# Optimization experiments

Hardware: AMD Instinct MI355X
Metric: run time of the kernel (lower is better)

Reference implementation:

```python
import jax, jax.numpy as jnp
import numpy as np
from jax import lax

SEQ_LEN = 12
E = 64        # embedding_dim
HD = 128      # h_dim
G = 32        # number of scenes (seq_start_end rows)
P = 32        # pedestrians per scene
B = G * P     # total batch
BOT = 1024    # bottleneck_dim
MLP = 1024    # mlp_dim
BN_S = 1.0 / np.sqrt(1.0 + 1e-5)  # eval BatchNorm1d with running mean 0 / var 1


def setup_inputs():
    key = jax.random.key(0)
    ks = jax.random.split(key, 32)
    r = lambda k, s, sc=0.1: (jax.random.normal(k, s, jnp.float32) * sc)
    starts = np.arange(G, dtype=np.int32) * P
    sse = jnp.asarray(np.stack([starts, starts + P], 1))
    return {
        'last_pos': r(ks[0], (B, 2), 1.0),
        'last_pos_rel': r(ks[1], (B, 2), 1.0),
        'h0': r(ks[2], (1, B, HD), 1.0),
        'c0': r(ks[3], (1, B, HD), 1.0),
        'vx': r(ks[4], (8, B), 1.0),
        'vy': r(ks[5], (8, B), 1.0),
        'agent_type': jax.random.uniform(ks[6], (8, B, 1), jnp.float32),
        'seq_start_end': sse,
        # decoder params
        'W_sp': r(ks[7], (2, E)), 'b_sp': r(ks[8], (E,)),
        'W_ih': r(ks[9], (E, 4 * HD)), 'W_hh': r(ks[10], (HD, 4 * HD)),
        'b_ih': r(ks[11], (4 * HD,)), 'b_hh': r(ks[12], (4 * HD,)),
        'W_h2p': r(ks[13], (HD, 2)), 'b_h2p': r(ks[14], (2,)),
        # AttenPoolNet params
        'Wp_sp': r(ks[15], (2, E)), 'bp_sp': r(ks[16], (E,)),
        'Wp_vel': r(ks[17], (2, E)), 'bp_vel': r(ks[18], (E,)),
        'Wp_at': r(ks[19], (6, E)), 'bp_at': r(ks[20], (E,)),
        'Wa1': r(ks[21], (E, MLP)), 'ba1': r(ks[22], (MLP,)),
        'Wa2': r(ks[23], (MLP, 1)), 'ba2': r(ks[24], (1,)),
        'Wm1': r(ks[25], (E + HD, 512)), 'bm1': r(ks[26], (512,)),
        'Wm2': r(ks[27], (512, BOT)), 'bm2': r(ks[28], (BOT,)),
        # decoder post-pool mlp: [h+bottleneck, mlp_dim, h]
        'Wd1': r(ks[29], (HD + BOT, MLP)), 'bd1': r(ks[30], (MLP,)),
        'Wd2': r(ks[31], (MLP, HD)), 'bd2': jnp.zeros((HD,), jnp.float32),
    }


def _bnrelu(x):
    # make_mlp: Linear -> BatchNorm1d (eval, mean 0 / var 1) -> ReLU
    return jax.nn.relu(x * BN_S)


def reference(last_pos, last_pos_rel, h0, c0, vx, vy, agent_type, seq_start_end,
              W_sp, b_sp, W_ih, W_hh, b_ih, b_hh, W_h2p, b_h2p,
              Wp_sp, bp_sp, Wp_vel, bp_vel, Wp_at, bp_at,
              Wa1, ba1, Wa2, ba2, Wm1, bm1, Wm2, bm2,
              Wd1, bd1, Wd2, bd2):
    g = seq_start_end.shape[0]
    p = last_pos.shape[0] // g

    at0 = agent_type[0].reshape(g, p, 1)               # agent_type[0,:,:] per group
    at_rep = jnp.repeat(at0, 6, axis=-1)               # .repeat(num_ped, 6) width expansion
    at_emb = at_rep @ Wp_at + bp_at                    # (g,p,E), index j (tiled over i)
    vel = jnp.stack([vx[-1], vy[-1]], -1).reshape(g, p, 2)
    _vel_emb = vel @ Wp_vel + bp_vel                   # computed in source, unused downstream

    def pool(h2d, pos):
        Hh = h2d.reshape(g, p, HD)
        pg = pos.reshape(g, p, 2)
        # rel[s,i,j] = pos[s,j] - pos[s,i]
        rel = pg[:, None, :, :] - pg[:, :, None, :]
        rel_emb = rel @ Wp_sp + bp_sp                  # (g,p,p,E)
        a = _bnrelu(rel_emb @ Wa1 + ba1)               # (g,p,p,MLP)
        s = _bnrelu(a @ Wa2 + ba2)                     # (g,p,p,1)
        w = jax.nn.softmax(s, axis=-1)                 # torch softmax(dim=1) over size-1 axis -> ones
        base = jnp.concatenate([Hh, at_emb], -1)       # (g,p,192), index j
        wt = base[:, None, :, :] * (0.05 * w)          # (g,p,p,192)
        m = _bnrelu(wt @ Wm1 + bm1)
        m = _bnrelu(m @ Wm2 + bm2)                     # (g,p,p,BOT)
        return m.max(axis=2).reshape(g * p, BOT)       # max over j per tile index i

    def lstm(x, h, c):
        gates = x @ W_ih + h @ W_hh + b_ih + b_hh
        i, f, gg, o = jnp.split(gates, 4, axis=-1)
        c = jax.nn.sigmoid(f) * c + jax.nn.sigmoid(i) * jnp.tanh(gg)
        h = jax.nn.sigmoid(o) * jnp.tanh(c)
        return h, c

    def step(carry, _):
        lp, di, h, c = carry
        h, c = lstm(di, h, c)
        rel = h @ W_h2p + b_h2p
        cur = rel + lp
        ph = pool(h, cur)
        dh = _bnrelu(jnp.concatenate([h, ph], -1) @ Wd1 + bd1)
        dh = _bnrelu(dh @ Wd2 + bd2)
        di = rel @ W_sp + b_sp
        return (cur, di, dh, c), rel

    init = (last_pos, last_pos_rel @ W_sp + b_sp, h0[0], c0[0])
    (lp, di, h, c), rels = lax.scan(step, init, None, length=SEQ_LEN)
    return rels, h[None]  # (seq_len,B,2), (1,B,HD)
```

## Files before the change

kernel.cpp:

```cpp
#include <hip/hip_runtime.h>
#include <math.h>

#define BN_SF 0.9999950000374997f

typedef __attribute__((ext_vector_type(8))) short short8v;
typedef __attribute__((ext_vector_type(4))) float float4v;

__device__ __forceinline__ float sigm(float x) { return 1.0f / (1.0f + expf(-x)); }

__device__ __forceinline__ short f2bf(float x) {
    unsigned u = __builtin_bit_cast(unsigned, x);
    unsigned r = (u + 0x7fffu + ((u >> 16) & 1u)) >> 16;
    return (short)r;
}
__device__ __forceinline__ float bf2f(short h) {
    unsigned u = ((unsigned)(unsigned short)h) << 16;
    return __builtin_bit_cast(float, u);
}

template <int K, int N>
__device__ __forceinline__ void cvtB8(const float* __restrict__ src, short* __restrict__ dst,
                                      float scale, int g) {
    const int KCN = K >> 5;
    int ntg = g / (KCN * 64);
    int rem = g - ntg * (KCN * 64);
    int kc = rem >> 6, lane = rem & 63;
    int n = ntg * 16 + (lane & 15);
    int k0 = kc * 32 + ((lane >> 4) << 3);
    short8v v;
#pragma unroll
    for (int j = 0; j < 8; ++j) v[j] = f2bf(scale * src[(size_t)(k0 + j) * N + n]);
    *(short8v*)(dst + (size_t)g * 8) = v;
}

struct SetupP {
    const float *Wm2, *Wd1, *Wd2, *Wm1, *Wih, *Whh, *Wpat, *bpat, *bm1;
    const float *lpr, *Wsp, *bsp, *c0;
    short *Wm2s, *Wd1f, *Wd2f, *Wm1f, *WgHi, *WgLo;
    float *uv, *di, *cbuf;
};

__global__ __launch_bounds__(256) void k_setup(SetupP p) {
    int gt = blockIdx.x * 256 + threadIdx.x;
    int stride = gridDim.x * 256;
    for (int g = gt; g < 512 * 1024 / 8; g += stride)  cvtB8<512, 1024>(p.Wm2, p.Wm2s, 1.f, g);
    for (int g = gt; g < 1152 * 1024 / 8; g += stride) cvtB8<1152, 1024>(p.Wd1, p.Wd1f, 1.f, g);
    for (int g = gt; g < 1024 * 128 / 8; g += stride)  cvtB8<1024, 128>(p.Wd2, p.Wd2f, 1.f, g);
    for (int g = gt; g < 128 * 512 / 8; g += stride)   cvtB8<128, 512>(p.Wm1, p.Wm1f, 0.05f, g);
    for (int g = gt; g < 192 * 512 / 8; g += stride) {
        int ntg = g / (6 * 64);
        int rem = g - ntg * (6 * 64);
        int kc = rem >> 6, lane = rem & 63;
        int n = ntg * 16 + (lane & 15);
        int k0 = kc * 32 + ((lane >> 4) << 3);
        short8v vh, vl;
#pragma unroll
        for (int j = 0; j < 8; ++j) {
            int k = k0 + j;
            float v = (k < 64) ? p.Wih[(size_t)k * 512 + n] : p.Whh[(size_t)(k - 64) * 512 + n];
            short hi = f2bf(v);
            vh[j] = hi; vl[j] = f2bf(v - bf2f(hi));
        }
        *(short8v*)(p.WgHi + (size_t)g * 8) = vh;
        *(short8v*)(p.WgLo + (size_t)g * 8) = vl;
    }
    for (int i = gt; i < 1024 * 64; i += stride) {
        int r = i >> 6, c = i & 63;
        p.di[i] = p.lpr[r * 2] * p.Wsp[c] + p.lpr[r * 2 + 1] * p.Wsp[64 + c] + p.bsp[c];
    }
    for (int i = gt; i < 1024 * 128; i += stride) p.cbuf[i] = p.c0[i];
    if (blockIdx.x == 0) {
        __shared__ float rw[64];
        int t = threadIdx.x;
        if (t < 64) { float s = 0.f; for (int k = 0; k < 6; ++k) s += p.Wpat[k * 64 + t]; rw[t] = s; }
        __syncthreads();
        for (int c = t; c < 512; c += 256) {
            float u = 0.f, v = 0.f;
            for (int e = 0; e < 64; ++e) {
                float wg = p.Wm1[(128 + e) * 512 + c];
                u += rw[e] * wg; v += p.bpat[e] * wg;
            }
            p.uv[c] = 0.05f * u; p.uv[512 + c] = 0.05f * v + p.bm1[c];
        }
    }
}

__global__ __launch_bounds__(512, 4) void k_step(
    const short* __restrict__ WgHi, const short* __restrict__ WgLo,
    const short* __restrict__ Wm1f, const short* __restrict__ Wd2f,
    const short* __restrict__ Wd1f,
    const float* __restrict__ bih, const float* __restrict__ bhh,
    const float* __restrict__ Whp, const float* __restrict__ bhp,
    const float* __restrict__ Wsp, const float* __restrict__ bsp,
    const float* __restrict__ bd1, const float* __restrict__ bd2,
    const float* __restrict__ at0, const float* __restrict__ uv,
    const float* __restrict__ h0,
    const float* __restrict__ phwp, const short* __restrict__ hf_in, int first,
    float* __restrict__ cbuf, float* __restrict__ di,
    short* __restrict__ hf_out, short* __restrict__ m1s,
    float* __restrict__ outrel) {
    __shared__ float sgu[16 * 512];
    __shared__ float sh[16][128];
    __shared__ float sdi[16][64];
    __shared__ float phws[1024];
    __shared__ short xfh[6 * 512];
    __shared__ short xfl[6 * 512];
    __shared__ short xm[4 * 512];
    __shared__ float sat[16];
    __shared__ float srel[16][2];
    short* dh1L = (short*)sgu;
    float* sg = sgu;

    int t = threadIdx.x, b = blockIdx.x;
    int l = t & 63, w = t >> 6;
    int s = b >> 1, mt = b & 1, r0 = b * 16;
    int rbase = (l >> 4) << 2;

    for (int i = t; i < 16 * 64; i += 512) sdi[i >> 6][i & 63] = di[r0 * 64 + i];
    if (t < 16) sat[t] = at0[r0 + t];

    if (first) {
        for (int i = t; i < 16 * 128; i += 512) sh[i >> 7][i & 127] = h0[r0 * 128 + i];
        __syncthreads();
    } else {
        for (int i = t; i < 1024; i += 512) {
            float v = bd1[i];
#pragma unroll
            for (int ct = 0; ct < 8; ++ct) v += phwp[(size_t)s * 8192 + ct * 1024 + i];
            phws[i] = v;
        }
        __syncthreads();
        short8v Ah[4];
#pragma unroll
        for (int kc = 0; kc < 4; ++kc)
            Ah[kc] = *(const short8v*)(hf_in + (size_t)b * 2048 + kc * 512 + l * 8);
#pragma unroll 1
        for (int q2 = 0; q2 < 4; ++q2) {
            short8v B[2][4];
#pragma unroll
            for (int qq = 0; qq < 2; ++qq)
#pragma unroll
                for (int kc = 0; kc < 4; ++kc)
                    B[qq][kc] = *(const short8v*)(Wd1f + (size_t)(w * 8 + q2 * 2 + qq) * 18432 + kc * 512 + l * 8);
            float4v acc2[2];
#pragma unroll
            for (int qq = 0; qq < 2; ++qq) {
                int col = (w * 8 + q2 * 2 + qq) * 16 + (l & 15);
                float pv = phws[col];
                acc2[qq] = (float4v){pv, pv, pv, pv};
            }
#pragma unroll
            for (int kc = 0; kc < 4; ++kc)
#pragma unroll
                for (int qq = 0; qq < 2; ++qq)
                    acc2[qq] = __builtin_amdgcn_mfma_f32_16x16x32_bf16(Ah[kc], B[qq][kc], acc2[qq], 0, 0, 0);
#pragma unroll
            for (int qq = 0; qq < 2; ++qq) {
                int col = (w * 8 + q2 * 2 + qq) * 16 + (l & 15);
                int kcD = col >> 5, jD = col & 7, lD = ((col & 31) >> 3) << 4;
#pragma unroll
                for (int r = 0; r < 4; ++r) {
                    float v = fmaxf(BN_SF * acc2[qq][r], 0.f);
                    dh1L[kcD * 512 + (rbase + r + lD) * 8 + jD] = f2bf(v);
                }
            }
        }
        __syncthreads();
        float4v hacc = {0.f, 0.f, 0.f, 0.f};
        const short* ap = dh1L + l * 8;
        const short* bp = Wd2f + (size_t)w * 16384 + l * 8;
#pragma unroll 1
        for (int kt = 0; kt < 4; ++kt) {
            short8v B[8], A[8];
#pragma unroll
            for (int kk = 0; kk < 8; ++kk) B[kk] = *(const short8v*)(bp + (kt * 8 + kk) * 512);
#pragma unroll
            for (int kk = 0; kk < 8; ++kk) A[kk] = *(const short8v*)(ap + (kt * 8 + kk) * 512);
#pragma unroll
            for (int kk = 0; kk < 8; ++kk)
                hacc = __builtin_amdgcn_mfma_f32_16x16x32_bf16(A[kk], B[kk], hacc, 0, 0, 0);
        }
        int col = w * 16 + (l & 15);
        float bb2 = bd2[col];
        __syncthreads();
#pragma unroll
        for (int r = 0; r < 4; ++r)
            sh[rbase + r][col] = fmaxf(BN_SF * (hacc[r] + bb2), 0.f);
        __syncthreads();
    }

    for (int i = t; i < 6 * 512; i += 512) {
        int pos = i & 511, kc = i >> 9;
        int ll = pos >> 3, j = pos & 7;
        int row = ll & 15, k = kc * 32 + ((ll >> 4) << 3) + j;
        float v = (k < 64) ? sdi[row][k] : sh[row][k - 64];
        short hi = f2bf(v);
        xfh[i] = hi;
        xfl[i] = f2bf(v - bf2f(hi));
    }
    __syncthreads();

    {
        float4v ga[4] = {{0,0,0,0},{0,0,0,0},{0,0,0,0},{0,0,0,0}};
#pragma unroll 1
        for (int kt = 0; kt < 3; ++kt) {
            short8v BH[2][4], BL[2][4], AH[2], AL[2];
#pragma unroll
            for (int kk = 0; kk < 2; ++kk) {
                int kc = kt * 2 + kk;
#pragma unroll
                for (int q = 0; q < 4; ++q) {
                    int nf = w * 4 + q;
                    BH[kk][q] = *(const short8v*)(WgHi + (size_t)nf * 3072 + kc * 512 + l * 8);
                    BL[kk][q] = *(const short8v*)(WgLo + (size_t)nf * 3072 + kc * 512 + l * 8);
                }
                AH[kk] = *(const short8v*)(&xfh[kc * 512 + l * 8]);
                AL[kk] = *(const short8v*)(&xfl[kc * 512 + l * 8]);
            }
#pragma unroll
            for (int kk = 0; kk < 2; ++kk)
#pragma unroll
                for (int q = 0; q < 4; ++q) {
                    ga[q] = __builtin_amdgcn_mfma_f32_16x16x32_bf16(AH[kk], BH[kk][q], ga[q], 0, 0, 0);
                    ga[q] = __builtin_amdgcn_mfma_f32_16x16x32_bf16(AH[kk], BL[kk][q], ga[q], 0, 0, 0);
                    ga[q] = __builtin_amdgcn_mfma_f32_16x16x32_bf16(AL[kk], BH[kk][q], ga[q], 0, 0, 0);
                }
        }
#pragma unroll
        for (int q = 0; q < 4; ++q) {
            int col = (w * 4 + q) * 16 + (l & 15);
            float bb = bih[col] + bhh[col];
#pragma unroll
            for (int r = 0; r < 4; ++r)
                sg[(rbase + r) * 512 + col] = ga[q][r] + bb;
        }
    }
    __syncthreads();

    for (int i = t; i < 16 * 128; i += 512) {
        int row = i >> 7, j = i & 127;
        float gi = sg[row * 512 + j], gf = sg[row * 512 + j + 128];
        float gg = sg[row * 512 + j + 256], go = sg[row * 512 + j + 384];
        float cn = sigm(gf) * cbuf[(r0 + row) * 128 + j] + sigm(gi) * tanhf(gg);
        float hn = sigm(go) * tanhf(cn);
        cbuf[(r0 + row) * 128 + j] = cn;
        sh[row][j] = hn;
    }
    __syncthreads();

    if (t < 32) {
        int row = t >> 1, d = t & 1;
        float s2 = bhp[d];
        for (int k = 0; k < 128; ++k) s2 += sh[row][k] * Whp[k * 2 + d];
        srel[row][d] = s2;
        outrel[(r0 + row) * 2 + d] = s2;
    }
    for (int i = t; i < 4 * 512; i += 512) {
        int pos = i & 511, kc = i >> 9;
        int ll = pos >> 3, j = pos & 7;
        int row = ll & 15, k = kc * 32 + ((ll >> 4) << 3) + j;
        short hv = f2bf(sh[row][k]);
        xm[i] = hv;
        hf_out[(size_t)b * 2048 + i] = hv;
    }
    __syncthreads();

    for (int i = t; i < 16 * 64; i += 512) {
        int row = i >> 6, c = i & 63;
        di[(r0 + row) * 64 + c] = srel[row][0] * Wsp[c] + srel[row][1] * Wsp[64 + c] + bsp[c];
    }

    {
        float4v ma[4] = {{0,0,0,0},{0,0,0,0},{0,0,0,0},{0,0,0,0}};
        short8v A[4], B[4][4];
#pragma unroll
        for (int kc = 0; kc < 4; ++kc) {
#pragma unroll
            for (int q = 0; q < 4; ++q)
                B[kc][q] = *(const short8v*)(Wm1f + (size_t)(w * 4 + q) * 2048 + kc * 512 + l * 8);
            A[kc] = *(const short8v*)(&xm[kc * 512 + l * 8]);
        }
#pragma unroll
        for (int kc = 0; kc < 4; ++kc)
#pragma unroll
            for (int q = 0; q < 4; ++q)
                ma[q] = __builtin_amdgcn_mfma_f32_16x16x32_bf16(A[kc], B[kc][q], ma[q], 0, 0, 0);
#pragma unroll
        for (int q = 0; q < 4; ++q) {
            int col = (w * 4 + q) * 16 + (l & 15);
            float uc = uv[col], vc = uv[512 + col];
#pragma unroll
            for (int r = 0; r < 4; ++r) {
                int rowC = rbase + r;
                float m1v = fmaxf(BN_SF * (ma[q][r] + sat[rowC] * uc + vc), 0.f);
                int kcD = col >> 5;
                int laneD = rowC + (((col & 31) >> 3) << 4);
                m1s[(size_t)s * 16384 + kcD * 1024 + mt * 512 + laneD * 8 + (col & 7)] = f2bf(m1v);
            }
        }
    }
}

__global__ __launch_bounds__(512, 4) void k_m2(const short* __restrict__ m1s,
                                               const short* __restrict__ Wm2s,
                                               const short* __restrict__ Wd1f,
                                               const float* __restrict__ bm2,
                                               float* __restrict__ phwp) {
    __shared__ short sphb[128];
    int t = threadIdx.x, l = t & 63, w = t >> 6;
    int s = blockIdx.x >> 3, ct = blockIdx.x & 7;

    {
        int nf = ct * 8 + w;
        const short* ap = m1s + (size_t)s * 16384 + l * 8;
        const short* bp = Wm2s + (size_t)nf * 8192 + l * 8;
        float4v acc0 = {0,0,0,0}, acc1 = {0,0,0,0};
#pragma unroll 1
        for (int kt = 0; kt < 4; ++kt) {
            short8v A0[4], A1[4], B[4];
#pragma unroll
            for (int kk = 0; kk < 4; ++kk) {
                int kc = kt * 4 + kk;
                B[kk] = *(const short8v*)(bp + kc * 512);
                A0[kk] = *(const short8v*)(ap + kc * 1024);
                A1[kk] = *(const short8v*)(ap + kc * 1024 + 512);
            }
#pragma unroll
            for (int kk = 0; kk < 4; ++kk) {
                acc0 = __builtin_amdgcn_mfma_f32_16x16x32_bf16(A0[kk], B[kk], acc0, 0, 0, 0);
                acc1 = __builtin_amdgcn_mfma_f32_16x16x32_bf16(A1[kk], B[kk], acc1, 0, 0, 0);
            }
        }
        float m = acc0[0];
#pragma unroll
        for (int ri = 1; ri < 4; ++ri) m = fmaxf(m, acc0[ri]);
#pragma unroll
        for (int ri = 0; ri < 4; ++ri) m = fmaxf(m, acc1[ri]);
        m = fmaxf(m, __shfl_xor(m, 16, 64));
        m = fmaxf(m, __shfl_xor(m, 32, 64));
        if (l < 16) {
            int col = nf * 16 + l;
            sphb[w * 16 + l] = f2bf(fmaxf(BN_SF * (m + bm2[col]), 0.f));
        }
    }
    __syncthreads();

    {
        short8v Ap[4];
#pragma unroll
        for (int kk = 0; kk < 4; ++kk)
            Ap[kk] = *(const short8v*)(sphb + kk * 32 + ((l >> 4) << 3));
#pragma unroll 1
        for (int q2 = 0; q2 < 4; ++q2) {
            short8v B[2][4];
#pragma unroll
            for (int qq = 0; qq < 2; ++qq)
#pragma unroll
                for (int kk = 0; kk < 4; ++kk)
                    B[qq][kk] = *(const short8v*)(Wd1f + (size_t)(w * 8 + q2 * 2 + qq) * 18432
                                                  + (size_t)(4 + ct * 4 + kk) * 512 + l * 8);
            float4v acc2[2] = {{0,0,0,0},{0,0,0,0}};
#pragma unroll
            for (int kk = 0; kk < 4; ++kk)
#pragma unroll
                for (int qq = 0; qq < 2; ++qq)
                    acc2[qq] = __builtin_amdgcn_mfma_f32_16x16x32_bf16(Ap[kk], B[qq][kk], acc2[qq], 0, 0, 0);
            if (l < 16) {
#pragma unroll
                for (int qq = 0; qq < 2; ++qq) {
                    int nf_p = w * 8 + q2 * 2 + qq;
                    phwp[(size_t)s * 8192 + ct * 1024 + nf_p * 16 + l] = acc2[qq][0];
                }
            }
        }
    }
}

__global__ __launch_bounds__(512, 4) void k_hfin(const short* __restrict__ Wd2f,
                                                 const short* __restrict__ Wd1f,
                                                 const float* __restrict__ bd1,
                                                 const float* __restrict__ bd2,
                                                 const float* __restrict__ phwp,
                                                 const short* __restrict__ hf,
                                                 float* __restrict__ outh) {
    __shared__ float phws[1024];
    __shared__ short dh1L[16384];
    int t = threadIdx.x, b = blockIdx.x;
    int l = t & 63, w = t >> 6;
    int s = b >> 1, rbase = (l >> 4) << 2;

    for (int i = t; i < 1024; i += 512) {
        float v = bd1[i];
#pragma unroll
        for (int ct = 0; ct < 8; ++ct) v += phwp[(size_t)s * 8192 + ct * 1024 + i];
        phws[i] = v;
    }
    __syncthreads();
    short8v Ah[4];
#pragma unroll
    for (int kc = 0; kc < 4; ++kc)
        Ah[kc] = *(const short8v*)(hf + (size_t)b * 2048 + kc * 512 + l * 8);
#pragma unroll 1
    for (int q2 = 0; q2 < 4; ++q2) {
        short8v B[2][4];
#pragma unroll
        for (int qq = 0; qq < 2; ++qq)
#pragma unroll
            for (int kc = 0; kc < 4; ++kc)
                B[qq][kc] = *(const short8v*)(Wd1f + (size_t)(w * 8 + q2 * 2 + qq) * 18432 + kc * 512 + l * 8);
        float4v acc2[2];
#pragma unroll
        for (int qq = 0; qq < 2; ++qq) {
            int col = (w * 8 + q2 * 2 + qq) * 16 + (l & 15);
            float pv = phws[col];
            acc2[qq] = (float4v){pv, pv, pv, pv};
        }
#pragma unroll
        for (int kc = 0; kc < 4; ++kc)
#pragma unroll
            for (int qq = 0; qq < 2; ++qq)
                acc2[qq] = __builtin_amdgcn_mfma_f32_16x16x32_bf16(Ah[kc], B[qq][kc], acc2[qq], 0, 0, 0);
#pragma unroll
        for (int qq = 0; qq < 2; ++qq) {
            int col = (w * 8 + q2 * 2 + qq) * 16 + (l & 15);
            int kcD = col >> 5, jD = col & 7, lD = ((col & 31) >> 3) << 4;
#pragma unroll
            for (int r = 0; r < 4; ++r) {
                float v = fmaxf(BN_SF * acc2[qq][r], 0.f);
                dh1L[kcD * 512 + (rbase + r + lD) * 8 + jD] = f2bf(v);
            }
        }
    }
    __syncthreads();
    float4v hacc = {0.f, 0.f, 0.f, 0.f};
    const short* ap = dh1L + l * 8;
    const short* bp = Wd2f + (size_t)w * 16384 + l * 8;
#pragma unroll 1
    for (int kt = 0; kt < 4; ++kt) {
        short8v B[8], A[8];
#pragma unroll
        for (int kk = 0; kk < 8; ++kk) B[kk] = *(const short8v*)(bp + (kt * 8 + kk) * 512);
#pragma unroll
        for (int kk = 0; kk < 8; ++kk) A[kk] = *(const short8v*)(ap + (kt * 8 + kk) * 512);
#pragma unroll
        for (int kk = 0; kk < 8; ++kk)
            hacc = __builtin_amdgcn_mfma_f32_16x16x32_bf16(A[kk], B[kk], hacc, 0, 0, 0);
    }
    int col = w * 16 + (l & 15);
    float bb2 = bd2[col];
#pragma unroll
    for (int r = 0; r < 4; ++r)
        outh[(b * 16 + rbase + r) * 128 + col] = fmaxf(BN_SF * (hacc[r] + bb2), 0.f);
}

extern "C" void kernel_launch(void* const* d_in, const int* in_sizes, int n_in,
                              void* d_out, int out_size, void* d_ws, size_t ws_size,
                              hipStream_t stream) {
    const float* last_pos_rel = (const float*)d_in[1];
    const float* h0           = (const float*)d_in[2];
    const float* c0           = (const float*)d_in[3];
    const float* agent_type   = (const float*)d_in[6];
    const float* W_sp  = (const float*)d_in[8];
    const float* b_sp  = (const float*)d_in[9];
    const float* W_ih  = (const float*)d_in[10];
    const float* W_hh  = (const float*)d_in[11];
    const float* b_ih  = (const float*)d_in[12];
    const float* b_hh  = (const float*)d_in[13];
    const float* W_h2p = (const float*)d_in[14];
    const float* b_h2p = (const float*)d_in[15];
    const float* Wp_at = (const float*)d_in[20];
    const float* bp_at = (const float*)d_in[21];
    const float* Wm1   = (const float*)d_in[26];
    const float* bm1   = (const float*)d_in[27];
    const float* Wm2   = (const float*)d_in[28];
    const float* bm2   = (const float*)d_in[29];
    const float* Wd1   = (const float*)d_in[30];
    const float* bd1   = (const float*)d_in[31];
    const float* Wd2   = (const float*)d_in[32];
    const float* bd2   = (const float*)d_in[33];
    float* out = (float*)d_out;

    float* ws   = (float*)d_ws;
    float* uv   = ws;
    float* di   = uv + 1024;
    float* cbuf = di + 65536;
    float* phwp = cbuf + 131072;
    short* hf   = (short*)(phwp + 262144);
    short* m1s  = hf + 131072;
    short* Wm2s = m1s + 524288;
    short* Wd1f = Wm2s + 524288;
    short* Wd2f = Wd1f + 1179648;
    short* Wm1f = Wd2f + 131072;
    short* WgHi = Wm1f + 65536;
    short* WgLo = WgHi + 98304;

    SetupP sp;
    sp.Wm2 = Wm2; sp.Wd1 = Wd1; sp.Wd2 = Wd2; sp.Wm1 = Wm1;
    sp.Wih = W_ih; sp.Whh = W_hh; sp.Wpat = Wp_at; sp.bpat = bp_at; sp.bm1 = bm1;
    sp.lpr = last_pos_rel; sp.Wsp = W_sp; sp.bsp = b_sp; sp.c0 = c0;
    sp.Wm2s = Wm2s; sp.Wd1f = Wd1f; sp.Wd2f = Wd2f;
    sp.Wm1f = Wm1f; sp.WgHi = WgHi; sp.WgLo = WgLo;
    sp.uv = uv; sp.di = di; sp.cbuf = cbuf;

    k_setup<<<2048, 256, 0, stream>>>(sp);

    for (int t = 0; t < 12; ++t) {
        k_step<<<64, 512, 0, stream>>>(WgHi, WgLo, Wm1f, Wd2f, Wd1f,
                                       b_ih, b_hh, W_h2p, b_h2p, W_sp, b_sp,
                                       bd1, bd2, agent_type, uv, h0,
                                       phwp, hf, (t == 0) ? 1 : 0,
                                       cbuf, di, hf, m1s, out + (size_t)t * 2048);
        k_m2<<<256, 512, 0, stream>>>(m1s, Wm2s, Wd1f, bm2, phwp);
    }
    k_hfin<<<64, 512, 0, stream>>>(Wd2f, Wd1f, bd1, bd2, phwp, hf, out + 24576);
}
```

Baseline: 372.9 us.

## Fold decoder input projection into LSTM gate weights and tile setup conversions

Precomputes W_sp·W_ih and the combined bias, so the LSTM input contribution becomes a rank-2 update from the previous rel output rather than a 64-wide split-bf16 MFMA over a stored di buffer. This removes the di workspace round trip and one third of the gate GEMM K-loop. The setup kernel is restructured to convert weights through a shared-memory tile with one tile per block for coalesced reads, and the h2p reduction is spread across 256 threads using shuffles. The input path is now computed in fp32 rather than hi/lo bf16, which slightly changes rounding.

```diff
diff --git a/kernel.cpp b/kernel.cpp
--- a/kernel.cpp
+++ b/kernel.cpp
@@ -18,96 +18,102 @@
     return __builtin_bit_cast(float, u);
 }
 
-template <int K, int N>
-__device__ __forceinline__ void cvtB8(const float* __restrict__ src, short* __restrict__ dst,
-                                      float scale, int g) {
-    const int KCN = K >> 5;
-    int ntg = g / (KCN * 64);
-    int rem = g - ntg * (KCN * 64);
-    int kc = rem >> 6, lane = rem & 63;
-    int n = ntg * 16 + (lane & 15);
-    int k0 = kc * 32 + ((lane >> 4) << 3);
-    short8v v;
-#pragma unroll
-    for (int j = 0; j < 8; ++j) v[j] = f2bf(scale * src[(size_t)(k0 + j) * N + n]);
-    *(short8v*)(dst + (size_t)g * 8) = v;
-}
-
 struct SetupP {
-    const float *Wm2, *Wd1, *Wd2, *Wm1, *Wih, *Whh, *Wpat, *bpat, *bm1;
-    const float *lpr, *Wsp, *bsp, *c0;
-    short *Wm2s, *Wd1f, *Wd2f, *Wm1f, *WgHi, *WgLo;
-    float *uv, *di, *cbuf;
+    const float *Wm2, *Wd1, *Wd2, *Wm1, *Wih, *Whh, *Wpat, *bpat, *bm1, *c0;
+    const float *Wsp, *bsp, *bih, *bhh;
+    short *Wm2s, *Wd1f, *Wd2f, *Wm1f, *WghHi, *WghLo;
+    float *uv, *cbuf, *fc;
 };
 
 __global__ __launch_bounds__(256) void k_setup(SetupP p) {
-    int gt = blockIdx.x * 256 + threadIdx.x;
-    int stride = gridDim.x * 256;
-    for (int g = gt; g < 512 * 1024 / 8; g += stride)  cvtB8<512, 1024>(p.Wm2, p.Wm2s, 1.f, g);
-    for (int g = gt; g < 1152 * 1024 / 8; g += stride) cvtB8<1152, 1024>(p.Wd1, p.Wd1f, 1.f, g);
-    for (int g = gt; g < 1024 * 128 / 8; g += stride)  cvtB8<1024, 128>(p.Wd2, p.Wd2f, 1.f, g);
-    for (int g = gt; g < 128 * 512 / 8; g += stride)   cvtB8<128, 512>(p.Wm1, p.Wm1f, 0.05f, g);
-    for (int g = gt; g < 192 * 512 / 8; g += stride) {
-        int ntg = g / (6 * 64);
-        int rem = g - ntg * (6 * 64);
-        int kc = rem >> 6, lane = rem & 63;
-        int n = ntg * 16 + (lane & 15);
-        int k0 = kc * 32 + ((lane >> 4) << 3);
+    __shared__ float tile[32][65];
+    __shared__ float rw2[64], su[4][64], sv[4][64];
+    int b = blockIdx.x, t = threadIdx.x;
+
+    if (b < 960) {
+        const float* src; short* dst; short* dst2 = nullptr;
+        int K, N, tm; float scale = 1.f;
+        if (b < 256)      { src = p.Wm2; dst = p.Wm2s; K = 512;  N = 1024; tm = b; }
+        else if (b < 832) { src = p.Wd1; dst = p.Wd1f; K = 1152; N = 1024; tm = b - 256; }
+        else if (b < 896) { src = p.Wd2; dst = p.Wd2f; K = 1024; N = 128;  tm = b - 832; }
+        else if (b < 928) { src = p.Wm1; dst = p.Wm1f; K = 128;  N = 512;  tm = b - 896; scale = 0.05f; }
+        else              { src = p.Whh; dst = p.WghHi; dst2 = p.WghLo; K = 128; N = 512; tm = b - 928; }
+        int tiles_n = N >> 6;
+        int kt = tm / tiles_n, nt = tm - kt * tiles_n;
+        for (int i = t; i < 2048; i += 256) {
+            int r = i >> 6, c = i & 63;
+            tile[r][c] = scale * src[(size_t)(kt * 32 + r) * N + nt * 64 + c];
+        }
+        __syncthreads();
+        int lane = t & 63, ntgl = t >> 6;
+        int ntg = nt * 4 + ntgl;
+        size_t off = (size_t)ntg * ((K >> 5) * 512) + (size_t)kt * 512 + lane * 8;
+        int kl = (lane >> 4) << 3, nl = ntgl * 16 + (lane & 15);
         short8v vh, vl;
 #pragma unroll
         for (int j = 0; j < 8; ++j) {
-            int k = k0 + j;
-            float v = (k < 64) ? p.Wih[(size_t)k * 512 + n] : p.Whh[(size_t)(k - 64) * 512 + n];
+            float v = tile[kl + j][nl];
             short hi = f2bf(v);
             vh[j] = hi; vl[j] = f2bf(v - bf2f(hi));
         }
-        *(short8v*)(p.WgHi + (size_t)g * 8) = vh;
-        *(short8v*)(p.WgLo + (size_t)g * 8) = vl;
-    }
-    for (int i = gt; i < 1024 * 64; i += stride) {
-        int r = i >> 6, c = i & 63;
-        p.di[i] = p.lpr[r * 2] * p.Wsp[c] + p.lpr[r * 2 + 1] * p.Wsp[64 + c] + p.bsp[c];
-    }
-    for (int i = gt; i < 1024 * 128; i += stride) p.cbuf[i] = p.c0[i];
-    if (blockIdx.x == 0) {
-        __shared__ float rw[64];
-        int t = threadIdx.x;
-        if (t < 64) { float s = 0.f; for (int k = 0; k < 6; ++k) s += p.Wpat[k * 64 + t]; rw[t] = s; }
-        __syncthreads();
+        *(short8v*)(dst + off) = vh;
+        if (dst2) *(short8v*)(dst2 + off) = vl;
+    } else {
+        int i0 = (b - 960) * 256 + t;
+        ((float4*)p.cbuf)[i0] = ((const float4*)p.c0)[i0];
+        ((float4*)p.cbuf)[i0 + 16384] = ((const float4*)p.c0)[i0 + 16384];
+    }
+
+    if (b < 8) {
+        int lane = t & 63, seg = t >> 6;
+        if (t < 64) { float s = 0.f; for (int k = 0; k < 6; ++k) s += p.Wpat[k * 64 + t]; rw2[t] = s; }
+        __syncthreads();
+        int c = b * 64 + lane;
+        float u = 0.f, v = 0.f;
+        for (int e = seg * 16; e < seg * 16 + 16; ++e) {
+            float wg = p.Wm1[(size_t)(128 + e) * 512 + c];
+            u += rw2[e] * wg; v += p.bpat[e] * wg;
+        }
+        su[seg][lane] = u; sv[seg][lane] = v;
+        __syncthreads();
+        if (seg == 0) {
+            u = su[0][lane] + su[1][lane] + su[2][lane] + su[3][lane];
+            v = sv[0][lane] + sv[1][lane] + sv[2][lane] + sv[3][lane];
+            p.uv[c] = 0.05f * u; p.uv[512 + c] = 0.05f * v + p.bm1[c];
+        }
+    }
+    if (b == 8) {
         for (int c = t; c < 512; c += 256) {
-            float u = 0.f, v = 0.f;
+            float f0 = 0.f, f1 = 0.f, cc = 0.f;
             for (int e = 0; e < 64; ++e) {
-                float wg = p.Wm1[(128 + e) * 512 + c];
-                u += rw[e] * wg; v += p.bpat[e] * wg;
-            }
-            p.uv[c] = 0.05f * u; p.uv[512 + c] = 0.05f * v + p.bm1[c];
+                float wv = p.Wih[(size_t)e * 512 + c];
+                f0 += p.Wsp[e] * wv; f1 += p.Wsp[64 + e] * wv; cc += p.bsp[e] * wv;
+            }
+            p.fc[c] = f0; p.fc[512 + c] = f1; p.fc[1024 + c] = cc + p.bih[c] + p.bhh[c];
         }
     }
 }
 
 __global__ __launch_bounds__(512, 4) void k_step(
-    const short* __restrict__ WgHi, const short* __restrict__ WgLo,
+    const short* __restrict__ WghHi, const short* __restrict__ WghLo,
     const short* __restrict__ Wm1f, const short* __restrict__ Wd2f,
     const short* __restrict__ Wd1f,
-    const float* __restrict__ bih, const float* __restrict__ bhh,
     const float* __restrict__ Whp, const float* __restrict__ bhp,
-    const float* __restrict__ Wsp, const float* __restrict__ bsp,
     const float* __restrict__ bd1, const float* __restrict__ bd2,
     const float* __restrict__ at0, const float* __restrict__ uv,
-    const float* __restrict__ h0,
+    const float* __restrict__ fc,
+    const float* __restrict__ h0, const float* __restrict__ relsrc,
     const float* __restrict__ phwp, const short* __restrict__ hf_in, int first,
-    float* __restrict__ cbuf, float* __restrict__ di,
-    short* __restrict__ hf_out, short* __restrict__ m1s,
-    float* __restrict__ outrel) {
+    float* __restrict__ cbuf, short* __restrict__ hf_out,
+    short* __restrict__ m1s, float* __restrict__ outrel) {
     __shared__ float sgu[16 * 512];
     __shared__ float sh[16][128];
-    __shared__ float sdi[16][64];
     __shared__ float phws[1024];
-    __shared__ short xfh[6 * 512];
-    __shared__ short xfl[6 * 512];
+    __shared__ short xfh[4 * 512];
+    __shared__ short xfl[4 * 512];
     __shared__ short xm[4 * 512];
+    __shared__ float srelp[16][2];
     __shared__ float sat[16];
-    __shared__ float srel[16][2];
     short* dh1L = (short*)sgu;
     float* sg = sgu;
 
@@ -116,8 +122,8 @@
     int s = b >> 1, mt = b & 1, r0 = b * 16;
     int rbase = (l >> 4) << 2;
 
-    for (int i = t; i < 16 * 64; i += 512) sdi[i >> 6][i & 63] = di[r0 * 64 + i];
     if (t < 16) sat[t] = at0[r0 + t];
+    if (t < 32) { int row = t >> 1, d = t & 1; srelp[row][d] = relsrc[(r0 + row) * 2 + d]; }
 
     if (first) {
         for (int i = t; i < 16 * 128; i += 512) sh[i >> 7][i & 127] = h0[r0 * 128 + i];
@@ -189,11 +195,11 @@
         __syncthreads();
     }
 
-    for (int i = t; i < 6 * 512; i += 512) {
+    for (int i = t; i < 4 * 512; i += 512) {
         int pos = i & 511, kc = i >> 9;
         int ll = pos >> 3, j = pos & 7;
-        int row = ll & 15, k = kc * 32 + ((ll >> 4) << 3) + j;
-        float v = (k < 64) ? sdi[row][k] : sh[row][k - 64];
+        int row = ll & 15, kh = kc * 32 + ((ll >> 4) << 3) + j;
+        float v = sh[row][kh];
         short hi = f2bf(v);
         xfh[i] = hi;
         xfl[i] = f2bf(v - bf2f(hi));
@@ -201,21 +207,29 @@
     __syncthreads();
 
     {
-        float4v ga[4] = {{0,0,0,0},{0,0,0,0},{0,0,0,0},{0,0,0,0}};
-#pragma unroll 1
-        for (int kt = 0; kt < 3; ++kt) {
+        float4v ga[4];
+#pragma unroll
+        for (int q = 0; q < 4; ++q) {
+            int col = (w * 4 + q) * 16 + (l & 15);
+            float f0 = fc[col], f1 = fc[512 + col], cc = fc[1024 + col];
+#pragma unroll
+            for (int r = 0; r < 4; ++r)
+                ga[q][r] = srelp[rbase + r][0] * f0 + srelp[rbase + r][1] * f1 + cc;
+        }
+#pragma unroll 1
+        for (int kt = 0; kt < 2; ++kt) {
             short8v BH[2][4], BL[2][4], AH[2], AL[2];
 #pragma unroll
             for (int kk = 0; kk < 2; ++kk) {
-                int kc = kt * 2 + kk;
+                int kcx = kt * 2 + kk;
 #pragma unroll
                 for (int q = 0; q < 4; ++q) {
                     int nf = w * 4 + q;
-                    BH[kk][q] = *(const short8v*)(WgHi + (size_t)nf * 3072 + kc * 512 + l * 8);
-                    BL[kk][q] = *(const short8v*)(WgLo + (size_t)nf * 3072 + kc * 512 + l * 8);
+                    BH[kk][q] = *(const short8v*)(WghHi + (size_t)nf * 2048 + kcx * 512 + l * 8);
+                    BL[kk][q] = *(const short8v*)(WghLo + (size_t)nf * 2048 + kcx * 512 + l * 8);
                 }
-                AH[kk] = *(const short8v*)(&xfh[kc * 512 + l * 8]);
-                AL[kk] = *(const short8v*)(&xfl[kc * 512 + l * 8]);
+                AH[kk] = *(const short8v*)(&xfh[kcx * 512 + l * 8]);
+                AL[kk] = *(const short8v*)(&xfl[kcx * 512 + l * 8]);
             }
 #pragma unroll
             for (int kk = 0; kk < 2; ++kk)
@@ -229,10 +243,9 @@
 #pragma unroll
         for (int q = 0; q < 4; ++q) {
             int col = (w * 4 + q) * 16 + (l & 15);
-            float bb = bih[col] + bhh[col];
 #pragma unroll
             for (int r = 0; r < 4; ++r)
-                sg[(rbase + r) * 512 + col] = ga[q][r] + bb;
+                sg[(rbase + r) * 512 + col] = ga[q][r];
         }
     }
     __syncthreads();
@@ -248,12 +261,16 @@
     }
     __syncthreads();
 
-    if (t < 32) {
-        int row = t >> 1, d = t & 1;
-        float s2 = bhp[d];
-        for (int k = 0; k < 128; ++k) s2 += sh[row][k] * Whp[k * 2 + d];
-        srel[row][d] = s2;
-        outrel[(r0 + row) * 2 + d] = s2;
+    if (t < 256) {
+        int row = t >> 4, d = (t >> 3) & 1, seg = t & 7;
+        float v = 0.f;
+#pragma unroll
+        for (int kk = 0; kk < 16; ++kk) {
+            int k = seg * 16 + kk;
+            v += sh[row][k] * Whp[k * 2 + d];
+        }
+        v += __shfl_xor(v, 1, 64); v += __shfl_xor(v, 2, 64); v += __shfl_xor(v, 4, 64);
+        if (seg == 0) outrel[(r0 + row) * 2 + d] = v + bhp[d];
     }
     for (int i = t; i < 4 * 512; i += 512) {
         int pos = i & 511, kc = i >> 9;
@@ -264,11 +281,6 @@
         hf_out[(size_t)b * 2048 + i] = hv;
     }
     __syncthreads();
-
-    for (int i = t; i < 16 * 64; i += 512) {
-        int row = i >> 6, c = i & 63;
-        di[(r0 + row) * 64 + c] = srel[row][0] * Wsp[c] + srel[row][1] * Wsp[64 + c] + bsp[c];
-    }
 
     {
         float4v ma[4] = {{0,0,0,0},{0,0,0,0},{0,0,0,0},{0,0,0,0}};
@@ -456,10 +468,10 @@
 extern "C" void kernel_launch(void* const* d_in, const int* in_sizes, int n_in,
                               void* d_out, int out_size, void* d_ws, size_t ws_size,
                               hipStream_t stream) {
-    const float* last_pos_rel = (const float*)d_in[1];
-    const float* h0           = (const float*)d_in[2];
-    const float* c0           = (const float*)d_in[3];
-    const float* agent_type   = (const float*)d_in[6];
+    const float* lpr   = (const float*)d_in[1];
+    const float* h0    = (const float*)d_in[2];
+    const float* c0    = (const float*)d_in[3];
+    const float* at0   = (const float*)d_in[6];
     const float* W_sp  = (const float*)d_in[8];
     const float* b_sp  = (const float*)d_in[9];
     const float* W_ih  = (const float*)d_in[10];
@@ -480,36 +492,36 @@
     const float* bd2   = (const float*)d_in[33];
     float* out = (float*)d_out;
 
-    float* ws   = (float*)d_ws;
-    float* uv   = ws;
-    float* di   = uv + 1024;
-    float* cbuf = di + 65536;
-    float* phwp = cbuf + 131072;
-    short* hf   = (short*)(phwp + 262144);
-    short* m1s  = hf + 131072;
-    short* Wm2s = m1s + 524288;
-    short* Wd1f = Wm2s + 524288;
-    short* Wd2f = Wd1f + 1179648;
-    short* Wm1f = Wd2f + 131072;
-    short* WgHi = Wm1f + 65536;
-    short* WgLo = WgHi + 98304;
+    float* ws    = (float*)d_ws;
+    float* uv    = ws;
+    float* fc    = uv + 1024;
+    float* cbuf  = fc + 1536;
+    float* phwp  = cbuf + 131072;
+    short* hf    = (short*)(phwp + 262144);
+    short* m1s   = hf + 131072;
+    short* Wm2s  = m1s + 524288;
+    short* Wd1f  = Wm2s + 524288;
+    short* Wd2f  = Wd1f + 1179648;
+    short* Wm1f  = Wd2f + 131072;
+    short* WghHi = Wm1f + 65536;
+    short* WghLo = WghHi + 65536;
 
     SetupP sp;
     sp.Wm2 = Wm2; sp.Wd1 = Wd1; sp.Wd2 = Wd2; sp.Wm1 = Wm1;
     sp.Wih = W_ih; sp.Whh = W_hh; sp.Wpat = Wp_at; sp.bpat = bp_at; sp.bm1 = bm1;
-    sp.lpr = last_pos_rel; sp.Wsp = W_sp; sp.bsp = b_sp; sp.c0 = c0;
+    sp.c0 = c0; sp.Wsp = W_sp; sp.bsp = b_sp; sp.bih = b_ih; sp.bhh = b_hh;
     sp.Wm2s = Wm2s; sp.Wd1f = Wd1f; sp.Wd2f = Wd2f;
-    sp.Wm1f = Wm1f; sp.WgHi = WgHi; sp.WgLo = WgLo;
-    sp.uv = uv; sp.di = di; sp.cbuf = cbuf;
-
-    k_setup<<<2048, 256, 0, stream>>>(sp);
+    sp.Wm1f = Wm1f; sp.WghHi = WghHi; sp.WghLo = WghLo;
+    sp.uv = uv; sp.cbuf = cbuf; sp.fc = fc;
+
+    k_setup<<<1024, 256, 0, stream>>>(sp);
 
     for (int t = 0; t < 12; ++t) {
-        k_step<<<64, 512, 0, stream>>>(WgHi, WgLo, Wm1f, Wd2f, Wd1f,
-                                       b_ih, b_hh, W_h2p, b_h2p, W_sp, b_sp,
-                                       bd1, bd2, agent_type, uv, h0,
-                                       phwp, hf, (t == 0) ? 1 : 0,
-                                       cbuf, di, hf, m1s, out + (size_t)t * 2048);
+        const float* relsrc = (t == 0) ? lpr : (out + (size_t)(t - 1) * 2048);
+        k_step<<<64, 512, 0, stream>>>(WghHi, WghLo, Wm1f, Wd2f, Wd1f,
+                                       W_h2p, b_h2p, bd1, bd2, at0, uv, fc,
+                                       h0, relsrc, phwp, hf, (t == 0) ? 1 : 0,
+                                       cbuf, hf, m1s, out + (size_t)t * 2048);
         k_m2<<<256, 512, 0, stream>>>(m1s, Wm2s, Wd1f, bm2, phwp);
     }
     k_hfin<<<64, 512, 0, stream>>>(Wd2f, Wd1f, bd1, bd2, phwp, hf, out + 24576);
```

After: 328.3 us, median of 2. 1.14x faster.
